# Performance work log

Hardware: AMD Instinct MI355X
Metric: run time of the kernel (lower is better)

## Reference

```python
import jax, jax.numpy as jnp
import numpy as np


def setup_inputs() -> dict:
    key = jax.random.key(0)
    ks = jax.random.split(key, 10)
    B, S, H = 8192, 8, 256
    SD, PD, AD = 9, 2, 7

    def lin(k, fan_in, shape):
        bound = 1.0 / np.sqrt(fan_in)
        return jax.random.uniform(k, shape, jnp.float32, -bound, bound)

    return {
        "state": jax.random.normal(ks[0], (B, SD), jnp.float32),
        "proprio": jax.random.normal(ks[1], (B, PD), jnp.float32),
        "target_pos": jax.random.normal(ks[2], (B, 3), jnp.float32),
        "noise": jax.random.normal(ks[3], (S, B, AD), jnp.float32),
        # action_proposal: Linear(11,H) -> ReLU -> Linear(H,7) -> Tanh
        "pw1": lin(ks[4], SD + PD, (SD + PD, H)),
        "pb1": jnp.zeros((H,), jnp.float32),
        "pw2": lin(ks[5], H, (H, AD)),
        "pb2": jnp.zeros((AD,), jnp.float32),
        # forward_model: Linear(16,H) -> ReLU -> Linear(H,H) -> ReLU -> Linear(H,9)
        "w1": lin(ks[6], SD + AD, (SD + AD, H)),
        "b1": jnp.zeros((H,), jnp.float32),
        "w2": lin(ks[7], H, (H, H)),
        "b2": jnp.zeros((H,), jnp.float32),
        "w3": lin(ks[8], H, (H, SD)),
        "b3": jnp.zeros((SD,), jnp.float32),
        "horizon": 4,
    }


def reference(state, proprio, target_pos, noise, pw1, pb1, pw2, pb2,
              w1, b1, w2, b2, w3, b3, horizon):
    # action proposal
    x = jnp.concatenate([state, proprio], axis=-1)          # (B, 11)
    base_action = jnp.tanh(jax.nn.relu(x @ pw1 + pb1) @ pw2 + pb2)  # (B, 7)

    # candidates for all samples at once (vectorizes the num_samples loop)
    cand = jnp.clip(base_action[None] + 0.2 * noise, -1.0, 1.0)      # (S, B, 7)

    S = cand.shape[0]
    sim0 = jnp.broadcast_to(state[None], (S,) + state.shape)         # (S, B, 9)

    def step(carry, _):
        sim, total = carry
        inp = jnp.concatenate([sim, cand], axis=-1)                  # (S, B, 16)
        h = jax.nn.relu(inp @ w1 + b1)
        h = jax.nn.relu(h @ w2 + b2)
        sim = h @ w3 + b3                                            # (S, B, 9)
        cost = jnp.sum((sim[..., :3] - target_pos[None]) ** 2, axis=-1)  # (S, B)
        return (sim, total + cost), None

    total0 = jnp.zeros(cand.shape[:2], jnp.float32)
    (_, total_cost), _ = jax.lax.scan(step, (sim0, total0), None, length=horizon)

    # masked best-cost update with strict '<' against +inf == first-argmin over samples
    best = jnp.argmin(total_cost, axis=0)                            # (B,)
    best_actions = jnp.take_along_axis(cand, best[None, :, None], axis=0)[0]  # (B, 7)
    return best_actions
```

## Files before the change

kernel.cpp:

```cpp
#include <hip/hip_runtime.h>
#include <math.h>

#define NSD 9
#define NPD 2
#define NAD 7
#define NH  256
#define NIN 16
#define LOSCALE 2048.0f
#define LOINV   (1.0f / 2048.0f)
#define NPACKB 152
#define SLICE 10240

typedef _Float16 half8 __attribute__((ext_vector_type(8)));
typedef float    floatx4 __attribute__((ext_vector_type(4)));


__device__ __forceinline__ void stage16(const _Float16* g, _Float16* l)
{
    __builtin_amdgcn_global_load_lds(
        (const __attribute__((address_space(1))) void*)g,
        (__attribute__((address_space(3))) void*)l, 16, 0, 0);
}

__global__ __launch_bounds__(256) void k_prep(
    const float* __restrict__ w1, const float* __restrict__ b1,
    const float* __restrict__ w2, const float* __restrict__ w3,
    _Float16* __restrict__ pc, _Float16* __restrict__ p3,
    const float* __restrict__ state, const float* __restrict__ proprio,
    const float* __restrict__ noise, const float* __restrict__ pw1,
    const float* __restrict__ pb1, const float* __restrict__ pw2,
    const float* __restrict__ pb2, float* __restrict__ cand, int B)
{
    const int bid = blockIdx.x;
    if (bid < NPACKB) {
        if (threadIdx.x >= 64) return;
        const int lane = threadIdx.x;
        const int q = lane >> 4, ln = lane & 15;
        half8 hv, lv;
        if (bid < 16) {
            const int t = bid;
            const int c = 32*(t>>1) + 8*(ln>>2) + 4*(t&1) + (ln&3);
#pragma unroll
            for (int j = 0; j < 8; ++j) {
                const int k = 8*q + j;
                const float x = (k < NIN) ? w1[k*NH + c]
                                          : (k == NIN ? b1[c] : 0.0f);
                const _Float16 h = (_Float16)x;
                hv[j] = h; lv[j] = (_Float16)((x - (float)h) * LOSCALE);
            }
            const size_t off = 8192 + (size_t)(t & 1) * 1024;
            _Float16* d0 = pc + (size_t)(t >> 1) * SLICE + off;
            _Float16* d1 = pc + (size_t)(8 + (t >> 1)) * SLICE + off;
            *(half8*)&d0[lane*8]       = hv;
            *(half8*)&d0[512 + lane*8] = lv;
            *(half8*)&d1[lane*8]       = hv;
            *(half8*)&d1[512 + lane*8] = lv;
            return;
        }
        _Float16* dst;
        if (bid < 144) {
            const int idx = bid - 16, t = idx >> 3, kc = idx & 7;
            const int c = 32*(t>>1) + 8*(ln>>2) + 4*(t&1) + (ln&3);
#pragma unroll
            for (int j = 0; j < 8; ++j) {
                const int k = kc*32 + 8*q + j;
                const float x = w2[k*NH + c];
                const _Float16 h = (_Float16)x;
                hv[j] = h; lv[j] = (_Float16)((x - (float)h) * LOSCALE);
            }
            dst = pc + (size_t)((t >> 3) * 8 + kc) * SLICE + (size_t)(t & 7) * 1024;
        } else {
            const int kc = bid - 144;
#pragma unroll
            for (int j = 0; j < 8; ++j) {
                const int k = kc*32 + 8*q + j;
                const float x = (ln < NSD) ? w3[k*NSD + ln] : 0.0f;
                const _Float16 h = (_Float16)x;
                hv[j] = h; lv[j] = (_Float16)((x - (float)h) * LOSCALE);
            }
            dst = p3 + (size_t)kc * 1024;
        }
        *(half8*)&dst[lane*8]       = hv;
        *(half8*)&dst[512 + lane*8] = lv;
        return;
    }

    const int pbid = bid - NPACKB;
    const int wave = threadIdx.x >> 6;
    const int lane = threadIdx.x & 63;
    const int b = pbid * 4 + wave;
    if (b >= B) return;

    float x[11];
#pragma unroll
    for (int k = 0; k < 9; ++k) x[k] = state[b * NSD + k];
    x[9]  = proprio[b * NPD + 0];
    x[10] = proprio[b * NPD + 1];

    float hc[4];
#pragma unroll
    for (int i = 0; i < 4; ++i) {
        const int c = lane + 64 * i;
        float acc = pb1[c];
#pragma unroll
        for (int k = 0; k < 11; ++k) acc = fmaf(x[k], pw1[k * NH + c], acc);
        hc[i] = fmaxf(acc, 0.0f);
    }

    float base[7];
#pragma unroll
    for (int j = 0; j < 7; ++j) {
        float p = 0.0f;
#pragma unroll
        for (int i = 0; i < 4; ++i)
            p = fmaf(hc[i], pw2[(lane + 64 * i) * NAD + j], p);
#pragma unroll
        for (int off = 32; off >= 1; off >>= 1) p += __shfl_xor(p, off, 64);
        base[j] = tanhf(p + pb2[j]);
    }

    if (lane < 8 * NAD) {
        const int s = lane / NAD, j = lane % NAD;
        float bj = base[0];
#pragma unroll
        for (int jj = 1; jj < 7; ++jj) if (j == jj) bj = base[jj];
        float v = bj + 0.2f * noise[((size_t)s * B + b) * NAD + j];
        v = fminf(fmaxf(v, -1.0f), 1.0f);
        cand[((size_t)s * B + b) * NAD + j] = v;
    }
}

__global__ __launch_bounds__(256, 3) void k_rollout(
    const float* __restrict__ state, const float* __restrict__ target,
    const float* __restrict__ cand,
    const _Float16* __restrict__ pc, const _Float16* __restrict__ p3,
    const float* __restrict__ b2, const float* __restrict__ b3,
    const int* __restrict__ hor_ptr, float* __restrict__ cost, int B)
{
    __shared__ _Float16 sb[2][SLICE];
    __shared__ float inpL[4][16][20];
    __shared__ float b2L[NH];

    const int tid  = threadIdx.x;
    const int wv   = tid >> 6;
    const int lane = tid & 63;
    const int q = lane >> 4, ln = lane & 15;
    const int chunk = blockIdx.x * 4 + wv;
    const int p0 = chunk * 16;
    const int s  = p0 / B;
    const int b0 = p0 % B;
    const int horizon = *hor_ptr;

    auto STAGE = [&](int buf, int sidx) {
        const _Float16* gbase = pc + (size_t)sidx * SLICE + tid * 8;
        _Float16* lbase = &sb[buf][wv * 512];
#pragma unroll
        for (int i = 0; i < 5; ++i)
            stage16(gbase + i * 2048, lbase + i * 2048);
    };

    b2L[tid] = b2[tid];
    if (q == 0) {
        float* row = &inpL[wv][ln][0];
        const int b = b0 + ln;
#pragma unroll
        for (int k = 0; k < NSD; ++k) row[k] = state[b * NSD + k];
#pragma unroll
        for (int j = 0; j < NAD; ++j)
            row[NSD + j] = cand[((size_t)s * B + b) * NAD + j];
        row[16] = 1.0f; row[17] = 0.0f; row[18] = 0.0f; row[19] = 0.0f;
    }
    float tg[3] = {0.0f, 0.0f, 0.0f};
    if (q == 0) {
#pragma unroll
        for (int r = 0; r < 3; ++r) tg[r] = target[(b0 + ln) * 3 + r];
    }
    float b3v[4];
#pragma unroll
    for (int r = 0; r < 4; ++r) {
        const int f = q * 4 + r;
        b3v[r] = (f < NSD) ? b3[f] : 0.0f;
    }
    float costAcc = 0.0f;

    STAGE(0, 0);
    asm volatile("s_waitcnt vmcnt(0)" ::: "memory");
    __syncthreads();
    int cur = 0, sidx = 0;

    const floatx4 z4 = {0.0f, 0.0f, 0.0f, 0.0f};

    for (int h = 0; h < horizon; ++h) {
        const float* row = &inpL[wv][ln][0];
        float4 fa = {0, 0, 0, 0}, fb = {0, 0, 0, 0};
        if (q < 3) fa = *(const float4*)&row[8 * q];
        if (q < 2) fb = *(const float4*)&row[8 * q + 4];
        half8 bh, bl;
        {
            const float vv[8] = {fa.x, fa.y, fa.z, fa.w, fb.x, fb.y, fb.z, fb.w};
#pragma unroll
            for (int j = 0; j < 8; ++j) {
                const _Float16 hh = (_Float16)vv[j];
                bh[j] = hh;
                bl[j] = (_Float16)((vv[j] - (float)hh) * LOSCALE);
            }
        }

        floatx4 D1 = z4, D2 = z4;

#pragma unroll
        for (int pass = 0; pass < 2; ++pass) {
            floatx4 C1[8], C2[8];
#pragma unroll
            for (int tt = 0; tt < 8; ++tt) { C1[tt] = z4; C2[tt] = z4; }

            for (int kc = 0; kc < 8; ++kc) {
                const int nsidx = (sidx + 1) & 15;
                STAGE(cur ^ 1, nsidx);

                half8 h1h, h1l;
                {
                    const half8 a1h0 = *(const half8*)&sb[cur][8192 + lane*8];
                    const half8 a1l0 = *(const half8*)&sb[cur][8192 + 512 + lane*8];
                    const half8 a1h1 = *(const half8*)&sb[cur][8192 + 1024 + lane*8];
                    const half8 a1l1 = *(const half8*)&sb[cur][8192 + 1536 + lane*8];
                    floatx4 c1t = __builtin_amdgcn_mfma_f32_16x16x32_f16(a1h0, bh, z4, 0, 0, 0);
                    floatx4 c2t = __builtin_amdgcn_mfma_f32_16x16x32_f16(a1h0, bl, z4, 0, 0, 0);
                    c2t = __builtin_amdgcn_mfma_f32_16x16x32_f16(a1l0, bh, c2t, 0, 0, 0);
#pragma unroll
                    for (int r = 0; r < 4; ++r) {
                        const float v = fmaxf(fmaf(c2t[r], LOINV, c1t[r]), 0.0f);
                        const _Float16 hh = (_Float16)v;
                        h1h[r] = hh;
                        h1l[r] = (_Float16)((v - (float)hh) * LOSCALE);
                    }
                    c1t = __builtin_amdgcn_mfma_f32_16x16x32_f16(a1h1, bh, z4, 0, 0, 0);
                    c2t = __builtin_amdgcn_mfma_f32_16x16x32_f16(a1h1, bl, z4, 0, 0, 0);
                    c2t = __builtin_amdgcn_mfma_f32_16x16x32_f16(a1l1, bh, c2t, 0, 0, 0);
#pragma unroll
                    for (int r = 0; r < 4; ++r) {
                        const float v = fmaxf(fmaf(c2t[r], LOINV, c1t[r]), 0.0f);
                        const _Float16 hh = (_Float16)v;
                        h1h[4 + r] = hh;
                        h1l[4 + r] = (_Float16)((v - (float)hh) * LOSCALE);
                    }
                }

#pragma unroll
                for (int tt = 0; tt < 8; ++tt) {
                    const half8 a2h = *(const half8*)&sb[cur][tt * 1024 + lane * 8];
                    const half8 a2l = *(const half8*)&sb[cur][tt * 1024 + 512 + lane * 8];
                    C1[tt] = __builtin_amdgcn_mfma_f32_16x16x32_f16(a2h, h1h, C1[tt], 0, 0, 0);
                    C2[tt] = __builtin_amdgcn_mfma_f32_16x16x32_f16(a2h, h1l, C2[tt], 0, 0, 0);
                    C2[tt] = __builtin_amdgcn_mfma_f32_16x16x32_f16(a2l, h1h, C2[tt], 0, 0, 0);
                }

                __syncthreads();
                cur ^= 1;
                sidx = nsidx;
            }

            half8 h2h, h2l;
#pragma unroll
            for (int tt = 0; tt < 8; ++tt) {
                const int t = pass * 8 + tt;
                const float4 bb = *(const float4*)&b2L[32*(t>>1) + 8*q + 4*(t&1)];
                const float bbv[4] = {bb.x, bb.y, bb.z, bb.w};
#pragma unroll
                for (int r = 0; r < 4; ++r) {
                    const float v = fmaxf(C1[tt][r] + LOINV * C2[tt][r] + bbv[r], 0.0f);
                    const _Float16 hh = (_Float16)v;
                    h2h[(tt & 1) * 4 + r] = hh;
                    h2l[(tt & 1) * 4 + r] = (_Float16)((v - (float)hh) * LOSCALE);
                }
                if (tt & 1) {
                    const int kc2 = t >> 1;
                    const half8 a3h = *(const half8*)&p3[(size_t)kc2 * 1024 + lane*8];
                    const half8 a3l = *(const half8*)&p3[(size_t)kc2 * 1024 + 512 + lane*8];
                    D1 = __builtin_amdgcn_mfma_f32_16x16x32_f16(a3h, h2h, D1, 0, 0, 0);
                    D2 = __builtin_amdgcn_mfma_f32_16x16x32_f16(a3h, h2l, D2, 0, 0, 0);
                    D2 = __builtin_amdgcn_mfma_f32_16x16x32_f16(a3l, h2h, D2, 0, 0, 0);
                }
            }
        }

        float v[4];
#pragma unroll
        for (int r = 0; r < 4; ++r)
            v[r] = D1[r] + LOINV * D2[r] + b3v[r];

        if (q == 0) {
            const float d0 = v[0] - tg[0], d1 = v[1] - tg[1], d2 = v[2] - tg[2];
            costAcc += d0 * d0 + d1 * d1 + d2 * d2;
        }
        if (q < 2) {
            const float4 w4 = {v[0], v[1], v[2], v[3]};
            *(float4*)&inpL[wv][ln][4 * q] = w4;
        } else if (q == 2) {
            inpL[wv][ln][8] = v[0];
        }
        asm volatile("s_waitcnt lgkmcnt(0)" ::: "memory");
    }

    if (q == 0) cost[(size_t)s * B + b0 + ln] = costAcc;
}

__global__ __launch_bounds__(256) void k_select(
    const float* __restrict__ cost, const float* __restrict__ cand,
    float* __restrict__ out, int B, int S)
{
    const int b = blockIdx.x * 256 + threadIdx.x;
    if (b >= B) return;
    float best = cost[b];
    int bs = 0;
    for (int s = 1; s < S; ++s) {
        const float c = cost[(size_t)s * B + b];
        if (c < best) { best = c; bs = s; }
    }
#pragma unroll
    for (int j = 0; j < NAD; ++j)
        out[b * NAD + j] = cand[((size_t)bs * B + b) * NAD + j];
}

extern "C" void kernel_launch(void* const* d_in, const int* in_sizes, int n_in,
                              void* d_out, int out_size, void* d_ws, size_t ws_size,
                              hipStream_t stream)
{
    const float* state   = (const float*)d_in[0];
    const float* proprio = (const float*)d_in[1];
    const float* target  = (const float*)d_in[2];
    const float* noise   = (const float*)d_in[3];
    const float* pw1     = (const float*)d_in[4];
    const float* pb1     = (const float*)d_in[5];
    const float* pw2     = (const float*)d_in[6];
    const float* pb2     = (const float*)d_in[7];
    const float* w1      = (const float*)d_in[8];
    const float* b1      = (const float*)d_in[9];
    const float* w2      = (const float*)d_in[10];
    const float* b2      = (const float*)d_in[11];
    const float* w3      = (const float*)d_in[12];
    const float* b3      = (const float*)d_in[13];
    const int*   horizon = (const int*)d_in[14];

    const int B = in_sizes[0] / NSD;
    const int S = in_sizes[3] / (B * NAD);

    float* cand = (float*)d_ws;
    float* cost = cand + (size_t)S * B * NAD;
    _Float16* pc = (_Float16*)(cost + (size_t)S * B);
    _Float16* p3 = pc + 16 * SLICE;
    float* out  = (float*)d_out;

    k_prep<<<dim3(NPACKB + (B + 3) / 4), dim3(256), 0, stream>>>(
        w1, b1, w2, w3, pc, p3,
        state, proprio, noise, pw1, pb1, pw2, pb2, cand, B);
    k_rollout<<<dim3((S * B) / 64), dim3(256), 0, stream>>>(
        state, target, cand, pc, p3, b2, b3, horizon, cost, B);
    k_select<<<dim3((B + 255) / 256), dim3(256), 0, stream>>>(
        cost, cand, out, B, S);
}
```

Baseline: 255.4 us.

## Split layer-2 output into four passes to cut LDS and raise occupancy

The layer-2 output columns are now processed in four passes of 64 instead of two passes of 128. This shrinks each staged weight slice and the per-pass accumulator arrays, so LDS and VGPR use per block drop and launch bounds rise to four blocks per CU. The cost is that layer 1 is recomputed twice as often (once per pass-chunk), and there are more slice stages and barriers.

Measured after the change: 478.6 us. +87.4%, slower.

```diff
diff --git a/kernel.cpp b/kernel.cpp
--- a/kernel.cpp
+++ b/kernel.cpp
@@ -9,7 +9,7 @@
 #define LOSCALE 2048.0f
 #define LOINV   (1.0f / 2048.0f)
 #define NPACKB 152
-#define SLICE 10240
+#define SLICE 6144
 
 typedef _Float16 half8 __attribute__((ext_vector_type(8)));
 typedef float    floatx4 __attribute__((ext_vector_type(4)));
@@ -48,13 +48,13 @@
                 const _Float16 h = (_Float16)x;
                 hv[j] = h; lv[j] = (_Float16)((x - (float)h) * LOSCALE);
             }
-            const size_t off = 8192 + (size_t)(t & 1) * 1024;
-            _Float16* d0 = pc + (size_t)(t >> 1) * SLICE + off;
-            _Float16* d1 = pc + (size_t)(8 + (t >> 1)) * SLICE + off;
-            *(half8*)&d0[lane*8]       = hv;
-            *(half8*)&d0[512 + lane*8] = lv;
-            *(half8*)&d1[lane*8]       = hv;
-            *(half8*)&d1[512 + lane*8] = lv;
+            const size_t off = 4096 + (size_t)(t & 1) * 1024;
+#pragma unroll
+            for (int p = 0; p < 4; ++p) {
+                _Float16* d = pc + (size_t)(p * 8 + (t >> 1)) * SLICE + off;
+                *(half8*)&d[lane*8]       = hv;
+                *(half8*)&d[512 + lane*8] = lv;
+            }
             return;
         }
         _Float16* dst;
@@ -68,7 +68,7 @@
                 const _Float16 h = (_Float16)x;
                 hv[j] = h; lv[j] = (_Float16)((x - (float)h) * LOSCALE);
             }
-            dst = pc + (size_t)((t >> 3) * 8 + kc) * SLICE + (size_t)(t & 7) * 1024;
+            dst = pc + (size_t)((t >> 2) * 8 + kc) * SLICE + (size_t)(t & 3) * 1024;
         } else {
             const int kc = bid - 144;
 #pragma unroll
@@ -130,7 +130,7 @@
     }
 }
 
-__global__ __launch_bounds__(256, 3) void k_rollout(
+__global__ __launch_bounds__(256, 4) void k_rollout(
     const float* __restrict__ state, const float* __restrict__ target,
     const float* __restrict__ cand,
     const _Float16* __restrict__ pc, const _Float16* __restrict__ p3,
@@ -155,7 +155,7 @@
         const _Float16* gbase = pc + (size_t)sidx * SLICE + tid * 8;
         _Float16* lbase = &sb[buf][wv * 512];
 #pragma unroll
-        for (int i = 0; i < 5; ++i)
+        for (int i = 0; i < 3; ++i)
             stage16(gbase + i * 2048, lbase + i * 2048);
     };
 
@@ -209,21 +209,21 @@
         floatx4 D1 = z4, D2 = z4;
 
 #pragma unroll
-        for (int pass = 0; pass < 2; ++pass) {
-            floatx4 C1[8], C2[8];
-#pragma unroll
-            for (int tt = 0; tt < 8; ++tt) { C1[tt] = z4; C2[tt] = z4; }
+        for (int pass = 0; pass < 4; ++pass) {
+            floatx4 C1[4], C2[4];
+#pragma unroll
+            for (int tq = 0; tq < 4; ++tq) { C1[tq] = z4; C2[tq] = z4; }
 
             for (int kc = 0; kc < 8; ++kc) {
-                const int nsidx = (sidx + 1) & 15;
+                const int nsidx = (sidx + 1) & 31;
                 STAGE(cur ^ 1, nsidx);
 
                 half8 h1h, h1l;
                 {
-                    const half8 a1h0 = *(const half8*)&sb[cur][8192 + lane*8];
-                    const half8 a1l0 = *(const half8*)&sb[cur][8192 + 512 + lane*8];
-                    const half8 a1h1 = *(const half8*)&sb[cur][8192 + 1024 + lane*8];
-                    const half8 a1l1 = *(const half8*)&sb[cur][8192 + 1536 + lane*8];
+                    const half8 a1h0 = *(const half8*)&sb[cur][4096 + lane*8];
+                    const half8 a1l0 = *(const half8*)&sb[cur][4096 + 512 + lane*8];
+                    const half8 a1h1 = *(const half8*)&sb[cur][4096 + 1024 + lane*8];
+                    const half8 a1l1 = *(const half8*)&sb[cur][4096 + 1536 + lane*8];
                     floatx4 c1t = __builtin_amdgcn_mfma_f32_16x16x32_f16(a1h0, bh, z4, 0, 0, 0);
                     floatx4 c2t = __builtin_amdgcn_mfma_f32_16x16x32_f16(a1h0, bl, z4, 0, 0, 0);
                     c2t = __builtin_amdgcn_mfma_f32_16x16x32_f16(a1l0, bh, c2t, 0, 0, 0);
@@ -247,12 +247,12 @@
                 }
 
 #pragma unroll
-                for (int tt = 0; tt < 8; ++tt) {
-                    const half8 a2h = *(const half8*)&sb[cur][tt * 1024 + lane * 8];
-                    const half8 a2l = *(const half8*)&sb[cur][tt * 1024 + 512 + lane * 8];
-                    C1[tt] = __builtin_amdgcn_mfma_f32_16x16x32_f16(a2h, h1h, C1[tt], 0, 0, 0);
-                    C2[tt] = __builtin_amdgcn_mfma_f32_16x16x32_f16(a2h, h1l, C2[tt], 0, 0, 0);
-                    C2[tt] = __builtin_amdgcn_mfma_f32_16x16x32_f16(a2l, h1h, C2[tt], 0, 0, 0);
+                for (int tq = 0; tq < 4; ++tq) {
+                    const half8 a2h = *(const half8*)&sb[cur][tq * 1024 + lane * 8];
+                    const half8 a2l = *(const half8*)&sb[cur][tq * 1024 + 512 + lane * 8];
+                    C1[tq] = __builtin_amdgcn_mfma_f32_16x16x32_f16(a2h, h1h, C1[tq], 0, 0, 0);
+                    C2[tq] = __builtin_amdgcn_mfma_f32_16x16x32_f16(a2h, h1l, C2[tq], 0, 0, 0);
+                    C2[tq] = __builtin_amdgcn_mfma_f32_16x16x32_f16(a2l, h1h, C2[tq], 0, 0, 0);
                 }
 
                 __syncthreads();
@@ -262,19 +262,19 @@
 
             half8 h2h, h2l;
 #pragma unroll
-            for (int tt = 0; tt < 8; ++tt) {
-                const int t = pass * 8 + tt;
+            for (int tq = 0; tq < 4; ++tq) {
+                const int t = pass * 4 + tq;
                 const float4 bb = *(const float4*)&b2L[32*(t>>1) + 8*q + 4*(t&1)];
                 const float bbv[4] = {bb.x, bb.y, bb.z, bb.w};
 #pragma unroll
                 for (int r = 0; r < 4; ++r) {
-                    const float v = fmaxf(C1[tt][r] + LOINV * C2[tt][r] + bbv[r], 0.0f);
+                    const float v = fmaxf(C1[tq][r] + LOINV * C2[tq][r] + bbv[r], 0.0f);
                     const _Float16 hh = (_Float16)v;
-                    h2h[(tt & 1) * 4 + r] = hh;
-                    h2l[(tt & 1) * 4 + r] = (_Float16)((v - (float)hh) * LOSCALE);
+                    h2h[(tq & 1) * 4 + r] = hh;
+                    h2l[(tq & 1) * 4 + r] = (_Float16)((v - (float)hh) * LOSCALE);
                 }
-                if (tt & 1) {
-                    const int kc2 = t >> 1;
+                if (tq & 1) {
+                    const int kc2 = pass * 2 + (tq >> 1);
                     const half8 a3h = *(const half8*)&p3[(size_t)kc2 * 1024 + lane*8];
                     const half8 a3l = *(const half8*)&p3[(size_t)kc2 * 1024 + 512 + lane*8];
                     D1 = __builtin_amdgcn_mfma_f32_16x16x32_f16(a3h, h2h, D1, 0, 0, 0);
@@ -348,7 +348,7 @@
     float* cand = (float*)d_ws;
     float* cost = cand + (size_t)S * B * NAD;
     _Float16* pc = (_Float16*)(cost + (size_t)S * B);
-    _Float16* p3 = pc + 16 * SLICE;
+    _Float16* p3 = pc + 32 * SLICE;
     float* out  = (float*)d_out;
 
     k_prep<<<dim3(NPACKB + (B + 3) / 4), dim3(256), 0, stream>>>(
```
